# Performance work log

Hardware: AMD Instinct MI355X
Metric: run time of the kernel (lower is better)

The kernel has to match this reference:

```python
import jax, jax.numpy as jnp
import numpy as np

N = 50000
E = 800000
DF = 8        # dim_feat
DH = 32       # dim_hidden = out_channels per head
H = 4         # heads
HC = H * DH
DE = 4        # edge_dim
DD = 256      # dim_dense
DO = 4        # dim_out
NL = 3        # num GAT layers
SLOPE = 0.2   # GAT negative_slope
NL_SLOPE = 0.01  # nn.LeakyReLU default


def setup_inputs() -> dict:
    key = jax.random.key(0)
    ks = jax.random.split(key, 32)
    p = lambda k, shp: (jax.random.normal(k, shp, dtype=jnp.float32) * 0.1)
    inp = {
        "x": jax.random.normal(ks[0], (N, DF), dtype=jnp.float32),
        "edge_index": jax.random.randint(ks[1], (2, E), 0, N, dtype=jnp.int64),
        "edge_attr": jax.random.normal(ks[2], (E, DE), dtype=jnp.float32),
        # layer 0 (in = DF)
        "Wl0": p(ks[3], (DF, HC)), "bl0": jnp.zeros((HC,), jnp.float32),
        "Wr0": p(ks[4], (DF, HC)), "br0": jnp.zeros((HC,), jnp.float32),
        "We0": p(ks[5], (DE, HC)),
        "att0": p(ks[6], (H, DH)),
        "bo0": jnp.zeros((DH,), jnp.float32),
        # layers 1..NL-1 stacked (in = DH)
        "Wl": p(ks[7], (NL - 1, DH, HC)), "bl": jnp.zeros((NL - 1, HC), jnp.float32),
        "Wr": p(ks[8], (NL - 1, DH, HC)), "br": jnp.zeros((NL - 1, HC), jnp.float32),
        "We": p(ks[9], (NL - 1, DE, HC)),
        "att": p(ks[10], (NL - 1, H, DH)),
        "bo": jnp.zeros((NL - 1, DH), jnp.float32),
        # MLP head
        "Wd1": p(ks[11], (DH, DD)), "bd1": jnp.zeros((DD,), jnp.float32),
        "Wd2": p(ks[12], (DD, DO)), "bd2": jnp.zeros((DO,), jnp.float32),
    }
    return inp


def gat_layer(x, src, dst, ea, Wl, bl, Wr, br, We, att, bo):
    # GATv2ConvNorm, concat=False, no self loops, eval (dropout off)
    xl = (x @ Wl + bl).reshape(-1, H, DH)   # source transform  [N,H,C]
    xr = (x @ Wr + br).reshape(-1, H, DH)   # target transform  [N,H,C]
    x_j = xl[src]                            # [E,H,C]
    x_i = xr[dst]                            # [E,H,C]
    ef = (ea @ We).reshape(-1, H, DH)        # [E,H,C]
    m = jax.nn.leaky_relu(x_i + x_j + ef, negative_slope=SLOPE)
    e = jnp.einsum('ehc,hc->eh', m, att)     # logits [E,H]
    # Lipschitz norm on logits
    ni = jnp.linalg.norm(x_i, axis=-1)       # [E,H]
    nj = jnp.linalg.norm(x_j, axis=-1)       # [E,H]
    mx = jax.ops.segment_max(nj, dst, num_segments=N)
    mx = jnp.where(jnp.isfinite(mx), mx, 0.0)  # empty groups -> 0 (torch include_self=False init)
    e = e / (4.0 * (ni + mx[dst]) + 1e-12)
    # scatter softmax over destination groups
    emax = jax.ops.segment_max(e, dst, num_segments=N)
    z = jnp.exp(e - emax[dst])
    s = jax.ops.segment_sum(z, dst, num_segments=N)
    alpha = z / (s[dst] + 1e-16)             # [E,H]
    out = jax.ops.segment_sum(alpha[..., None] * x_j, dst, num_segments=N)  # [N,H,C]
    return out.mean(axis=1) + bo             # concat=False -> mean over heads


def reference(x, edge_index, edge_attr, Wl0, bl0, Wr0, br0, We0, att0, bo0,
              Wl, bl, Wr, br, We, att, bo, Wd1, bd1, Wd2, bd2):
    src, dst = edge_index[0], edge_index[1]
    act = lambda a: jax.nn.leaky_relu(a, negative_slope=NL_SLOPE)
    h = act(gat_layer(x, src, dst, edge_attr, Wl0, bl0, Wr0, br0, We0, att0, bo0))
    for i in range(NL - 1):
        h = act(gat_layer(h, src, dst, edge_attr, Wl[i], bl[i], Wr[i], br[i], We[i], att[i], bo[i]))
    h = act(h @ Wd1 + bd1)
    return h @ Wd2 + bd2
```

## Files before the change

### kernel.cpp

```cpp
#include <hip/hip_runtime.h>
#include <hip/hip_fp16.h>
#include <math.h>

#define NN 50000
#define EE 800000
#define DFi 8
#define DHc 32
#define Hh 4
#define HCc 128
#define DEe 4
#define DDd 256
#define DOo 4

__global__ void detect_kernel(const unsigned int* __restrict__ w, int nwords, int* __restrict__ flag) {
    unsigned int acc = 0;
    for (int i = 2 * threadIdx.x + 1; i < nwords; i += 512) acc |= w[i];
    if (acc) atomicOr(flag, 1);
}

__global__ void convert_count_kernel(const void* __restrict__ buf, const int* __restrict__ flag,
                                     int* __restrict__ EI, int* __restrict__ counts) {
    int i = blockIdx.x * 256 + threadIdx.x;
    if (i >= 2 * EE) return;
    int v = (*flag) ? ((const int*)buf)[i] : (int)(((const long long*)buf)[i]);
    EI[i] = v;
    if (i >= EE) atomicAdd(&counts[v], 1);
}

__global__ void scanA_kernel(const int* __restrict__ counts, int* __restrict__ roff,
                             int* __restrict__ bsum, int M) {
    __shared__ int sd[256];
    int t = threadIdx.x;
    int idx = blockIdx.x * 256 + t;
    int v = (idx < M) ? counts[idx] : 0;
    sd[t] = v;
    __syncthreads();
    for (int off = 1; off < 256; off <<= 1) {
        int x = (t >= off) ? sd[t - off] : 0;
        __syncthreads();
        sd[t] += x;
        __syncthreads();
    }
    if (idx < M) roff[idx] = sd[t] - v;
    if (t == 255) bsum[blockIdx.x] = sd[255];
}

__global__ void scanB_kernel(const int* __restrict__ bsum, int* __restrict__ boff, int nb) {
    __shared__ int sd[256];
    int t = threadIdx.x;
    int v = (t < nb) ? bsum[t] : 0;
    sd[t] = v;
    __syncthreads();
    for (int off = 1; off < 256; off <<= 1) {
        int x = (t >= off) ? sd[t - off] : 0;
        __syncthreads();
        sd[t] += x;
        __syncthreads();
    }
    boff[t] = sd[t] - v;
}

__global__ void scanC_kernel(int* __restrict__ roff, const int* __restrict__ boff, int M) {
    int idx = blockIdx.x * 256 + threadIdx.x;
    if (idx < M) roff[idx] += boff[idx >> 8];
}

__global__ void fill_kernel(const int* __restrict__ EI, const int* __restrict__ roff,
                            int* __restrict__ cursor, long long* __restrict__ ce) {
    int e = blockIdx.x * 256 + threadIdx.x;
    if (e >= EE) return;
    int d = EI[EE + e];
    int s = EI[e];
    int pos = atomicAdd(&cursor[d], 1);
    ce[roff[d] + pos] = ((long long)e << 32) | (unsigned int)s;
}

__global__ __launch_bounds__(256) void sortw_kernel(const int* __restrict__ roff,
                                                    long long* __restrict__ ce,
                                                    const float4* __restrict__ EA4,
                                                    int* __restrict__ col,
                                                    __half* __restrict__ EAc) {
    const int n = blockIdx.x * 4 + (threadIdx.x >> 6);
    if (n >= NN) return;
    const int lane = threadIdx.x & 63;
    const int a = roff[n];
    const int d = roff[n + 1] - a;
    if (d <= 0) return;
    if (d <= 64) {
        int srcv = 0;
        unsigned key = 0xFFFFFFFFu;
        if (lane < d) {
            long long v = ce[a + lane];
            srcv = (int)(v & 0xffffffffLL);
            unsigned eid = (unsigned)(v >> 32);
            key = (eid << 6) | (unsigned)lane;
        }
#pragma unroll
        for (int k = 2; k <= 64; k <<= 1) {
#pragma unroll
            for (int j = k >> 1; j > 0; j >>= 1) {
                unsigned o = (unsigned)__shfl_xor((int)key, j);
                bool up = ((lane & k) == 0);
                bool lower = ((lane & j) == 0);
                unsigned mn = o < key ? o : key;
                unsigned mx = o < key ? key : o;
                key = (lower == up) ? mn : mx;
            }
        }
        if (lane < d) {
            int ol = (int)(key & 63u);
            int src = __shfl(srcv, ol);
            unsigned eid = key >> 6;
            col[a + lane] = src;
            float4 at = EA4[eid];
            __half2 lo = __floats2half2_rn(at.x, at.y);
            __half2 hi = __floats2half2_rn(at.z, at.w);
            uint2 pk;
            pk.x = *reinterpret_cast<unsigned int*>(&lo);
            pk.y = *reinterpret_cast<unsigned int*>(&hi);
            reinterpret_cast<uint2*>(EAc)[a + lane] = pk;
        }
    } else if (lane == 0) {
        for (int i2 = a + 1; i2 < a + d; i2++) {
            long long kk = ce[i2];
            int j2 = i2 - 1;
            while (j2 >= a && ce[j2] > kk) { ce[j2 + 1] = ce[j2]; j2--; }
            ce[j2 + 1] = kk;
        }
        for (int k = 0; k < d; k++) {
            long long key = ce[a + k];
            int src = (int)(key & 0xffffffffLL);
            int eid = (int)(key >> 32);
            col[a + k] = src;
            float4 at = EA4[eid];
            __half2 lo = __floats2half2_rn(at.x, at.y);
            __half2 hi = __floats2half2_rn(at.z, at.w);
            uint2 pk;
            pk.x = *reinterpret_cast<unsigned int*>(&lo);
            pk.y = *reinterpret_cast<unsigned int*>(&hi);
            reinterpret_cast<uint2*>(EAc)[a + k] = pk;
        }
    }
}

template <int IN>
__global__ __launch_bounds__(128) void transform_kernel(
    const float* __restrict__ Xin, const float* __restrict__ Wl, const float* __restrict__ bl,
    const float* __restrict__ Wr, const float* __restrict__ br,
    __half* __restrict__ XLh, float* __restrict__ XR,
    float* __restrict__ NLn, float* __restrict__ NRn) {
    const int t = threadIdx.x;
    float wl[IN], wr[IN];
#pragma unroll
    for (int k = 0; k < IN; k++) { wl[k] = Wl[k * HCc + t]; wr[k] = Wr[k * HCc + t]; }
    const float blv = bl[t], brv = br[t];
    __shared__ float xst[16][IN];
    const int nbeg = blockIdx.x * 16;
    for (int idx = t; idx < 16 * IN; idx += 128) {
        int r = idx / IN, cc = idx % IN;
        int n = nbeg + r;
        xst[r][cc] = (n < NN) ? Xin[n * IN + cc] : 0.f;
    }
    __syncthreads();
#pragma unroll 4
    for (int r = 0; r < 16; ++r) {
        int n = nbeg + r;
        if (n >= NN) break;
        float al = blv, ar = brv;
#pragma unroll
        for (int k = 0; k < IN; k++) { float xv = xst[r][k]; al = fmaf(xv, wl[k], al); ar = fmaf(xv, wr[k], ar); }
        XLh[n * HCc + t] = __float2half(al);
        XR[n * HCc + t] = ar;
        float sl = al * al, sr = ar * ar;
#pragma unroll
        for (int msk = 1; msk < 32; msk <<= 1) { sl += __shfl_xor(sl, msk); sr += __shfl_xor(sr, msk); }
        if ((t & 31) == 0) { NLn[n * 4 + (t >> 5)] = sqrtf(sl); NRn[n * 4 + (t >> 5)] = sqrtf(sr); }
    }
}

__device__ inline float4 h8tof4(unsigned int a, unsigned int b) {
    __half2 p0 = *reinterpret_cast<const __half2*>(&a);
    __half2 p1 = *reinterpret_cast<const __half2*>(&b);
    float2 lo = __half22float2(p0), hi = __half22float2(p1);
    return make_float4(lo.x, lo.y, hi.x, hi.y);
}

__global__ __launch_bounds__(256) void gat_kernel(
    const __half* __restrict__ XLh, const float* __restrict__ XR,
    const float* __restrict__ NLn, const float* __restrict__ NRn,
    const int* __restrict__ roff, const int* __restrict__ col,
    const __half* __restrict__ EAc, const float* __restrict__ We,
    const float* __restrict__ att, const float* __restrict__ bo,
    float* __restrict__ Hout) {
    const int lane = threadIdx.x & 63;
    const int c = lane & 15;
    const int g = lane >> 4;
    const int h = c >> 2;
    const int wslot = blockIdx.x * 4 + (threadIdx.x >> 6);
    const int NWn = gridDim.x * 16;

    const uint4*  XLu4 = reinterpret_cast<const uint4*>(XLh);
    const uint2*  EAu2 = reinterpret_cast<const uint2*>(EAc);
    const float4* XR4 = reinterpret_cast<const float4*>(XR);
    const float4* NL4 = reinterpret_cast<const float4*>(NLn);
    const float4* We4 = reinterpret_cast<const float4*>(We);
    const float4* at4 = reinterpret_cast<const float4*>(att);
    const float4* bo4 = reinterpret_cast<const float4*>(bo);
    float4* Ho4 = reinterpret_cast<float4*>(Hout);

    const float4 w0l = We4[2 * c],      w0h = We4[2 * c + 1];
    const float4 w1l = We4[32 + 2 * c], w1h = We4[32 + 2 * c + 1];
    const float4 w2l = We4[64 + 2 * c], w2h = We4[64 + 2 * c + 1];
    const float4 w3l = We4[96 + 2 * c], w3h = We4[96 + 2 * c + 1];
    const float4 atl = at4[2 * c],      ath = at4[2 * c + 1];

    for (int i = wslot * 4 + g; i < NN; i += NWn) {
        const int base = roff[i];
        const int deg = roff[i + 1] - base;

        if (deg == 0) {
            if (c < 8) {
                float4 b = bo4[c];
                float4 r;
                r.x = b.x > 0.f ? b.x : 0.01f * b.x;
                r.y = b.y > 0.f ? b.y : 0.01f * b.y;
                r.z = b.z > 0.f ? b.z : 0.01f * b.z;
                r.w = b.w > 0.f ? b.w : 0.01f * b.w;
                Ho4[i * 8 + c] = r;
            }
            continue;
        }

        const float4 xil = XR4[i * 32 + 2 * c], xih = XR4[i * 32 + 2 * c + 1];
        float srun = 0.f;
        float4 accl = make_float4(0.f, 0.f, 0.f, 0.f);
        float4 acch = make_float4(0.f, 0.f, 0.f, 0.f);

#define ISSUE(X_, E_, K)                                                          \
        {                                                                         \
            int kc = ((K) < deg) ? (K) : 0;                                       \
            int jx = col[base + kc];                                              \
            X_ = XLu4[jx * 16 + c];                                               \
            E_ = EAu2[base + kc];                                                 \
        }
        uint4 xA, xB, xC, xD, xE, xF;
        uint2 eA, eB, eC, eD, eE, eF;
        ISSUE(xA, eA, 0); ISSUE(xB, eB, 1); ISSUE(xC, eC, 2);
        ISSUE(xD, eD, 3); ISSUE(xE, eE, 4); ISSUE(xF, eF, 5);

        float4 mx = make_float4(0.f, 0.f, 0.f, 0.f);
        for (int k = c; k < deg; k += 16) {
            int j = col[base + k];
            float4 nj = NL4[j];
            mx.x = fmaxf(mx.x, nj.x); mx.y = fmaxf(mx.y, nj.y);
            mx.z = fmaxf(mx.z, nj.z); mx.w = fmaxf(mx.w, nj.w);
        }
#pragma unroll
        for (int msk = 1; msk < 16; msk <<= 1) {
            mx.x = fmaxf(mx.x, __shfl_xor(mx.x, msk));
            mx.y = fmaxf(mx.y, __shfl_xor(mx.y, msk));
            mx.z = fmaxf(mx.z, __shfl_xor(mx.z, msk));
            mx.w = fmaxf(mx.w, __shfl_xor(mx.w, msk));
        }
        float mxh = (h == 0) ? mx.x : (h == 1) ? mx.y : (h == 2) ? mx.z : mx.w;
        const float invD = 1.0f / (4.0f * (NRn[i * 4 + h] + mxh) + 1e-12f);

#define BODY(X_, E_, K)                                                           \
        {                                                                         \
            float4 a4 = h8tof4((E_).x, (E_).y);                                   \
            float4 xjl = h8tof4((X_).x, (X_).y);                                  \
            float4 xjh = h8tof4((X_).z, (X_).w);                                  \
            float e0 = a4.x * w0l.x; e0 = fmaf(a4.y, w1l.x, e0);                  \
            e0 = fmaf(a4.z, w2l.x, e0); e0 = fmaf(a4.w, w3l.x, e0);               \
            float e1 = a4.x * w0l.y; e1 = fmaf(a4.y, w1l.y, e1);                  \
            e1 = fmaf(a4.z, w2l.y, e1); e1 = fmaf(a4.w, w3l.y, e1);               \
            float e2 = a4.x * w0l.z; e2 = fmaf(a4.y, w1l.z, e2);                  \
            e2 = fmaf(a4.z, w2l.z, e2); e2 = fmaf(a4.w, w3l.z, e2);               \
            float e3 = a4.x * w0l.w; e3 = fmaf(a4.y, w1l.w, e3);                  \
            e3 = fmaf(a4.z, w2l.w, e3); e3 = fmaf(a4.w, w3l.w, e3);               \
            float e4 = a4.x * w0h.x; e4 = fmaf(a4.y, w1h.x, e4);                  \
            e4 = fmaf(a4.z, w2h.x, e4); e4 = fmaf(a4.w, w3h.x, e4);               \
            float e5 = a4.x * w0h.y; e5 = fmaf(a4.y, w1h.y, e5);                  \
            e5 = fmaf(a4.z, w2h.y, e5); e5 = fmaf(a4.w, w3h.y, e5);               \
            float e6 = a4.x * w0h.z; e6 = fmaf(a4.y, w1h.z, e6);                  \
            e6 = fmaf(a4.z, w2h.z, e6); e6 = fmaf(a4.w, w3h.z, e6);               \
            float e7 = a4.x * w0h.w; e7 = fmaf(a4.y, w1h.w, e7);                  \
            e7 = fmaf(a4.z, w2h.w, e7); e7 = fmaf(a4.w, w3h.w, e7);               \
            float s0 = xil.x + xjl.x + e0; s0 = s0 > 0.f ? s0 : 0.2f * s0;        \
            float s1 = xil.y + xjl.y + e1; s1 = s1 > 0.f ? s1 : 0.2f * s1;        \
            float s2 = xil.z + xjl.z + e2; s2 = s2 > 0.f ? s2 : 0.2f * s2;        \
            float s3 = xil.w + xjl.w + e3; s3 = s3 > 0.f ? s3 : 0.2f * s3;        \
            float s4 = xih.x + xjh.x + e4; s4 = s4 > 0.f ? s4 : 0.2f * s4;        \
            float s5 = xih.y + xjh.y + e5; s5 = s5 > 0.f ? s5 : 0.2f * s5;        \
            float s6 = xih.z + xjh.z + e6; s6 = s6 > 0.f ? s6 : 0.2f * s6;        \
            float s7 = xih.w + xjh.w + e7; s7 = s7 > 0.f ? s7 : 0.2f * s7;        \
            float pp = s0 * atl.x; pp = fmaf(s1, atl.y, pp);                      \
            pp = fmaf(s2, atl.z, pp); pp = fmaf(s3, atl.w, pp);                   \
            pp = fmaf(s4, ath.x, pp); pp = fmaf(s5, ath.y, pp);                   \
            pp = fmaf(s6, ath.z, pp); pp = fmaf(s7, ath.w, pp);                   \
            pp += __shfl_xor(pp, 1); pp += __shfl_xor(pp, 2);                     \
            float z = __expf(fminf(pp * invD, 60.f));                             \
            z = ((K) < deg) ? z : 0.f;                                            \
            srun += z;                                                            \
            accl.x = fmaf(z, xjl.x, accl.x);                                      \
            accl.y = fmaf(z, xjl.y, accl.y);                                      \
            accl.z = fmaf(z, xjl.z, accl.z);                                      \
            accl.w = fmaf(z, xjl.w, accl.w);                                      \
            acch.x = fmaf(z, xjh.x, acch.x);                                      \
            acch.y = fmaf(z, xjh.y, acch.y);                                      \
            acch.z = fmaf(z, xjh.z, acch.z);                                      \
            acch.w = fmaf(z, xjh.w, acch.w);                                      \
        }

        for (int k = 0; k < deg; k += 3) {
            uint4 nxD, nxE, nxF;
            uint2 neD, neE, neF;
            ISSUE(nxD, neD, k + 6);
            ISSUE(nxE, neE, k + 7);
            ISSUE(nxF, neF, k + 8);
            BODY(xA, eA, k);
            if (k + 1 < deg) BODY(xB, eB, k + 1);
            if (k + 2 < deg) BODY(xC, eC, k + 2);
            xA = xD; eA = eD; xB = xE; eB = eE; xC = xF; eC = eF;
            xD = nxD; eD = neD; xE = nxE; eE = neE; xF = nxF; eF = neF;
        }
#undef BODY
#undef ISSUE

        float inv = 1.0f / (srun + 1e-16f);
        float a0 = accl.x * inv, a1 = accl.y * inv, a2 = accl.z * inv, a3 = accl.w * inv;
        float a4_ = acch.x * inv, a5 = acch.y * inv, a6 = acch.z * inv, a7 = acch.w * inv;
        a0 += __shfl_xor(a0, 4); a0 += __shfl_xor(a0, 8);
        a1 += __shfl_xor(a1, 4); a1 += __shfl_xor(a1, 8);
        a2 += __shfl_xor(a2, 4); a2 += __shfl_xor(a2, 8);
        a3 += __shfl_xor(a3, 4); a3 += __shfl_xor(a3, 8);
        a4_ += __shfl_xor(a4_, 4); a4_ += __shfl_xor(a4_, 8);
        a5 += __shfl_xor(a5, 4); a5 += __shfl_xor(a5, 8);
        a6 += __shfl_xor(a6, 4); a6 += __shfl_xor(a6, 8);
        a7 += __shfl_xor(a7, 4); a7 += __shfl_xor(a7, 8);

        if (c < 4) {
            float4 bl_ = bo4[2 * c], bh_ = bo4[2 * c + 1];
            float4 rl, rh;
            rl.x = fmaf(0.25f, a0, bl_.x); rl.x = rl.x > 0.f ? rl.x : 0.01f * rl.x;
            rl.y = fmaf(0.25f, a1, bl_.y); rl.y = rl.y > 0.f ? rl.y : 0.01f * rl.y;
            rl.z = fmaf(0.25f, a2, bl_.z); rl.z = rl.z > 0.f ? rl.z : 0.01f * rl.z;
            rl.w = fmaf(0.25f, a3, bl_.w); rl.w = rl.w > 0.f ? rl.w : 0.01f * rl.w;
            rh.x = fmaf(0.25f, a4_, bh_.x); rh.x = rh.x > 0.f ? rh.x : 0.01f * rh.x;
            rh.y = fmaf(0.25f, a5, bh_.y); rh.y = rh.y > 0.f ? rh.y : 0.01f * rh.y;
            rh.z = fmaf(0.25f, a6, bh_.z); rh.z = rh.z > 0.f ? rh.z : 0.01f * rh.z;
            rh.w = fmaf(0.25f, a7, bh_.w); rh.w = rh.w > 0.f ? rh.w : 0.01f * rh.w;
            Ho4[i * 8 + 2 * c] = rl;
            Ho4[i * 8 + 2 * c + 1] = rh;
        }
    }
}

__global__ __launch_bounds__(256) void mlp_kernel(
    const float* __restrict__ Hin, const float* __restrict__ Wd1, const float* __restrict__ bd1,
    const float* __restrict__ Wd2, const float* __restrict__ bd2, float* __restrict__ out) {
    const int lane = threadIdx.x & 63;
    const int chunk = __builtin_amdgcn_readfirstlane(threadIdx.x >> 6);
    const int nb = blockIdx.x * 64;
    int node = nb + lane;
    int nclamp = node < NN ? node : NN - 1;

    float h[32];
    const float4* H4 = reinterpret_cast<const float4*>(Hin);
#pragma unroll
    for (int r = 0; r < 8; ++r) {
        float4 t = H4[nclamp * 8 + r];
        h[4 * r] = t.x; h[4 * r + 1] = t.y; h[4 * r + 2] = t.z; h[4 * r + 3] = t.w;
    }

    float o0 = 0.f, o1 = 0.f, o2 = 0.f, o3 = 0.f;
    const int dbase = chunk * 64;
    for (int t = 0; t < 4; ++t) {
        float acc[16];
#pragma unroll
        for (int j = 0; j < 16; ++j) acc[j] = bd1[dbase + t * 16 + j];
#pragma unroll 8
        for (int k = 0; k < 32; ++k) {
            const float* wr = Wd1 + k * DDd + dbase + t * 16;
#pragma unroll
            for (int j = 0; j < 16; ++j) acc[j] = fmaf(h[k], wr[j], acc[j]);
        }
#pragma unroll
        for (int j = 0; j < 16; ++j) {
            float hd = acc[j];
            hd = hd > 0.f ? hd : 0.01f * hd;
            int d = dbase + t * 16 + j;
            o0 = fmaf(hd, Wd2[d * 4 + 0], o0);
            o1 = fmaf(hd, Wd2[d * 4 + 1], o1);
            o2 = fmaf(hd, Wd2[d * 4 + 2], o2);
            o3 = fmaf(hd, Wd2[d * 4 + 3], o3);
        }
    }

    __shared__ float4 red[4][64];
    red[chunk][lane] = make_float4(o0, o1, o2, o3);
    __syncthreads();
    if (threadIdx.x < 64 && nb + (int)threadIdx.x < NN) {
        float4 r0 = red[0][threadIdx.x], r1 = red[1][threadIdx.x];
        float4 r2 = red[2][threadIdx.x], r3 = red[3][threadIdx.x];
        float4 o;
        o.x = r0.x + r1.x + r2.x + r3.x + bd2[0];
        o.y = r0.y + r1.y + r2.y + r3.y + bd2[1];
        o.z = r0.z + r1.z + r2.z + r3.z + bd2[2];
        o.w = r0.w + r1.w + r2.w + r3.w + bd2[3];
        reinterpret_cast<float4*>(out)[nb + threadIdx.x] = o;
    }
}

extern "C" void kernel_launch(void* const* d_in, const int* in_sizes, int n_in,
                              void* d_out, int out_size, void* d_ws, size_t ws_size,
                              hipStream_t stream) {
    const float* x    = (const float*)d_in[0];
    const void*  eraw = d_in[1];
    const float* ea   = (const float*)d_in[2];
    const float* Wl0  = (const float*)d_in[3];
    const float* bl0  = (const float*)d_in[4];
    const float* Wr0  = (const float*)d_in[5];
    const float* br0  = (const float*)d_in[6];
    const float* We0  = (const float*)d_in[7];
    const float* att0 = (const float*)d_in[8];
    const float* bo0  = (const float*)d_in[9];
    const float* Wl   = (const float*)d_in[10];
    const float* bl   = (const float*)d_in[11];
    const float* Wr   = (const float*)d_in[12];
    const float* br   = (const float*)d_in[13];
    const float* We   = (const float*)d_in[14];
    const float* att  = (const float*)d_in[15];
    const float* bo   = (const float*)d_in[16];
    const float* Wd1  = (const float*)d_in[17];
    const float* bd1  = (const float*)d_in[18];
    const float* Wd2  = (const float*)d_in[19];
    const float* bd2  = (const float*)d_in[20];
    float* out = (float*)d_out;

    char* p = (char*)d_ws;
    auto alloc = [&](size_t bytes) { void* r = (void*)p; p += (bytes + 255) & ~(size_t)255; return r; };
    int*       EI     = (int*)alloc((size_t)2 * EE * 4);
    int*       counts = (int*)alloc((size_t)(NN + 1) * 4);
    int*       roff   = (int*)alloc((size_t)(NN + 1) * 4);
    int*       bsum   = (int*)alloc(256 * 4);
    int*       boff   = (int*)alloc(256 * 4);
    int*       cursor = (int*)alloc((size_t)NN * 4);
    long long* ce     = (long long*)alloc((size_t)EE * 8);
    int*       col    = (int*)alloc((size_t)EE * 4);
    int*       flag   = (int*)alloc(256);
    __half*    XLh    = (__half*)alloc((size_t)NN * HCc * 2);
    __half*    EAc    = (__half*)alloc((size_t)EE * 4 * 2);
    float*     XRb    = (float*)alloc((size_t)NN * HCc * 4);
    float*     NLn    = (float*)alloc((size_t)NN * 4 * 4);
    float*     NRn    = (float*)alloc((size_t)NN * 4 * 4);
    float*     HA     = (float*)alloc((size_t)NN * DHc * 4);
    float*     HB     = (float*)alloc((size_t)NN * DHc * 4);

    (void)hipMemsetAsync(counts, 0, (size_t)(NN + 1) * 4, stream);
    (void)hipMemsetAsync(cursor, 0, (size_t)NN * 4, stream);
    (void)hipMemsetAsync(flag, 0, 4, stream);

    detect_kernel<<<1, 256, 0, stream>>>((const unsigned int*)eraw, 8192, flag);
    convert_count_kernel<<<(2 * EE + 255) / 256, 256, 0, stream>>>(eraw, flag, EI, counts);
    const int M = NN + 1;
    const int NBLK = (M + 255) / 256;
    scanA_kernel<<<NBLK, 256, 0, stream>>>(counts, roff, bsum, M);
    scanB_kernel<<<1, 256, 0, stream>>>(bsum, boff, NBLK);
    scanC_kernel<<<NBLK, 256, 0, stream>>>(roff, boff, M);
    fill_kernel<<<(EE + 255) / 256, 256, 0, stream>>>(EI, roff, cursor, ce);
    sortw_kernel<<<(NN + 3) / 4, 256, 0, stream>>>(roff, ce, (const float4*)ea, col, EAc);

    const int gT = (NN + 15) / 16;
    const int gG = 1563;

    transform_kernel<DFi><<<gT, 128, 0, stream>>>(x, Wl0, bl0, Wr0, br0, XLh, XRb, NLn, NRn);
    gat_kernel<<<gG, 256, 0, stream>>>(XLh, XRb, NLn, NRn, roff, col, EAc, We0, att0, bo0, HA);
    transform_kernel<DHc><<<gT, 128, 0, stream>>>(HA, Wl, bl, Wr, br, XLh, XRb, NLn, NRn);
    gat_kernel<<<gG, 256, 0, stream>>>(XLh, XRb, NLn, NRn, roff, col, EAc, We, att, bo, HB);
    transform_kernel<DHc><<<gT, 128, 0, stream>>>(HB, Wl + DHc * HCc, bl + HCc, Wr + DHc * HCc, br + HCc,
                                                  XLh, XRb, NLn, NRn);
    gat_kernel<<<gG, 256, 0, stream>>>(XLh, XRb, NLn, NRn, roff, col, EAc, We + DEe * HCc,
                                       att + Hh * DHc, bo + DHc, HA);
    mlp_kernel<<<(NN + 63) / 64, 256, 0, stream>>>(HA, Wd1, bd1, Wd2, bd2, out);
}
```

Before: 455.2 us.

## Sort nodes by in-degree and map one node per 16-lane group

```diff
diff --git a/kernel.cpp b/kernel.cpp
--- a/kernel.cpp
+++ b/kernel.cpp
@@ -143,6 +143,37 @@
     }
 }
 
+__global__ void dhist_kernel(const int* __restrict__ roff, int* __restrict__ dhist) {
+    int n = blockIdx.x * 256 + threadIdx.x;
+    if (n >= NN) return;
+    int d = roff[n + 1] - roff[n];
+    atomicAdd(&dhist[d < 255 ? d : 255], 1);
+}
+
+__global__ void dscan_kernel(const int* __restrict__ dhist, int* __restrict__ dcur) {
+    __shared__ int sd[256];
+    int t = threadIdx.x;
+    int v = dhist[t];
+    sd[t] = v;
+    __syncthreads();
+    for (int off = 1; off < 256; off <<= 1) {
+        int x = (t >= off) ? sd[t - off] : 0;
+        __syncthreads();
+        sd[t] += x;
+        __syncthreads();
+    }
+    dcur[t] = sd[t] - v;
+}
+
+__global__ void dscatter_kernel(const int* __restrict__ roff, int* __restrict__ dcur,
+                                int* __restrict__ perm) {
+    int n = blockIdx.x * 256 + threadIdx.x;
+    if (n >= NN) return;
+    int d = roff[n + 1] - roff[n];
+    int pos = atomicAdd(&dcur[d < 255 ? d : 255], 1);
+    perm[pos] = n;
+}
+
 template <int IN>
 __global__ __launch_bounds__(128) void transform_kernel(
     const float* __restrict__ Xin, const float* __restrict__ Wl, const float* __restrict__ bl,
@@ -189,15 +220,17 @@
     const __half* __restrict__ XLh, const float* __restrict__ XR,
     const float* __restrict__ NLn, const float* __restrict__ NRn,
     const int* __restrict__ roff, const int* __restrict__ col,
-    const __half* __restrict__ EAc, const float* __restrict__ We,
+    const __half* __restrict__ EAc, const int* __restrict__ perm,
+    const float* __restrict__ We,
     const float* __restrict__ att, const float* __restrict__ bo,
     float* __restrict__ Hout) {
     const int lane = threadIdx.x & 63;
     const int c = lane & 15;
     const int g = lane >> 4;
     const int h = c >> 2;
-    const int wslot = blockIdx.x * 4 + (threadIdx.x >> 6);
-    const int NWn = gridDim.x * 16;
+    const int slot = blockIdx.x * 16 + (threadIdx.x >> 6) * 4 + g;
+    if (slot >= NN) return;
+    const int i = perm[slot];
 
     const uint4*  XLu4 = reinterpret_cast<const uint4*>(XLh);
     const uint2*  EAu2 = reinterpret_cast<const uint2*>(EAc);
@@ -208,151 +241,149 @@
     const float4* bo4 = reinterpret_cast<const float4*>(bo);
     float4* Ho4 = reinterpret_cast<float4*>(Hout);
 
+    const int base = roff[i];
+    const int deg = roff[i + 1] - base;
+
+    if (deg == 0) {
+        if (c < 8) {
+            float4 b = bo4[c];
+            float4 r;
+            r.x = b.x > 0.f ? b.x : 0.01f * b.x;
+            r.y = b.y > 0.f ? b.y : 0.01f * b.y;
+            r.z = b.z > 0.f ? b.z : 0.01f * b.z;
+            r.w = b.w > 0.f ? b.w : 0.01f * b.w;
+            Ho4[i * 8 + c] = r;
+        }
+        return;
+    }
+
     const float4 w0l = We4[2 * c],      w0h = We4[2 * c + 1];
     const float4 w1l = We4[32 + 2 * c], w1h = We4[32 + 2 * c + 1];
     const float4 w2l = We4[64 + 2 * c], w2h = We4[64 + 2 * c + 1];
     const float4 w3l = We4[96 + 2 * c], w3h = We4[96 + 2 * c + 1];
     const float4 atl = at4[2 * c],      ath = at4[2 * c + 1];
 
-    for (int i = wslot * 4 + g; i < NN; i += NWn) {
-        const int base = roff[i];
-        const int deg = roff[i + 1] - base;
-
-        if (deg == 0) {
-            if (c < 8) {
-                float4 b = bo4[c];
-                float4 r;
-                r.x = b.x > 0.f ? b.x : 0.01f * b.x;
-                r.y = b.y > 0.f ? b.y : 0.01f * b.y;
-                r.z = b.z > 0.f ? b.z : 0.01f * b.z;
-                r.w = b.w > 0.f ? b.w : 0.01f * b.w;
-                Ho4[i * 8 + c] = r;
-            }
-            continue;
-        }
-
-        const float4 xil = XR4[i * 32 + 2 * c], xih = XR4[i * 32 + 2 * c + 1];
-        float srun = 0.f;
-        float4 accl = make_float4(0.f, 0.f, 0.f, 0.f);
-        float4 acch = make_float4(0.f, 0.f, 0.f, 0.f);
+    const float4 xil = XR4[i * 32 + 2 * c], xih = XR4[i * 32 + 2 * c + 1];
+    float srun = 0.f;
+    float4 accl = make_float4(0.f, 0.f, 0.f, 0.f);
+    float4 acch = make_float4(0.f, 0.f, 0.f, 0.f);
 
 #define ISSUE(X_, E_, K)                                                          \
-        {                                                                         \
-            int kc = ((K) < deg) ? (K) : 0;                                       \
-            int jx = col[base + kc];                                              \
-            X_ = XLu4[jx * 16 + c];                                               \
-            E_ = EAu2[base + kc];                                                 \
-        }
-        uint4 xA, xB, xC, xD, xE, xF;
-        uint2 eA, eB, eC, eD, eE, eF;
-        ISSUE(xA, eA, 0); ISSUE(xB, eB, 1); ISSUE(xC, eC, 2);
-        ISSUE(xD, eD, 3); ISSUE(xE, eE, 4); ISSUE(xF, eF, 5);
-
-        float4 mx = make_float4(0.f, 0.f, 0.f, 0.f);
-        for (int k = c; k < deg; k += 16) {
-            int j = col[base + k];
-            float4 nj = NL4[j];
-            mx.x = fmaxf(mx.x, nj.x); mx.y = fmaxf(mx.y, nj.y);
-            mx.z = fmaxf(mx.z, nj.z); mx.w = fmaxf(mx.w, nj.w);
-        }
-#pragma unroll
-        for (int msk = 1; msk < 16; msk <<= 1) {
-            mx.x = fmaxf(mx.x, __shfl_xor(mx.x, msk));
-            mx.y = fmaxf(mx.y, __shfl_xor(mx.y, msk));
-            mx.z = fmaxf(mx.z, __shfl_xor(mx.z, msk));
-            mx.w = fmaxf(mx.w, __shfl_xor(mx.w, msk));
-        }
-        float mxh = (h == 0) ? mx.x : (h == 1) ? mx.y : (h == 2) ? mx.z : mx.w;
-        const float invD = 1.0f / (4.0f * (NRn[i * 4 + h] + mxh) + 1e-12f);
+    {                                                                             \
+        int kc = ((K) < deg) ? (K) : 0;                                           \
+        int jx = col[base + kc];                                                  \
+        X_ = XLu4[jx * 16 + c];                                                   \
+        E_ = EAu2[base + kc];                                                     \
+    }
+    uint4 xA, xB, xC, xD, xE, xF;
+    uint2 eA, eB, eC, eD, eE, eF;
+    ISSUE(xA, eA, 0); ISSUE(xB, eB, 1); ISSUE(xC, eC, 2);
+    ISSUE(xD, eD, 3); ISSUE(xE, eE, 4); ISSUE(xF, eF, 5);
+
+    float4 mx = make_float4(0.f, 0.f, 0.f, 0.f);
+    for (int k = c; k < deg; k += 16) {
+        int j = col[base + k];
+        float4 nj = NL4[j];
+        mx.x = fmaxf(mx.x, nj.x); mx.y = fmaxf(mx.y, nj.y);
+        mx.z = fmaxf(mx.z, nj.z); mx.w = fmaxf(mx.w, nj.w);
+    }
+#pragma unroll
+    for (int msk = 1; msk < 16; msk <<= 1) {
+        mx.x = fmaxf(mx.x, __shfl_xor(mx.x, msk));
+        mx.y = fmaxf(mx.y, __shfl_xor(mx.y, msk));
+        mx.z = fmaxf(mx.z, __shfl_xor(mx.z, msk));
+        mx.w = fmaxf(mx.w, __shfl_xor(mx.w, msk));
+    }
+    float mxh = (h == 0) ? mx.x : (h == 1) ? mx.y : (h == 2) ? mx.z : mx.w;
+    const float invD = 1.0f / (4.0f * (NRn[i * 4 + h] + mxh) + 1e-12f);
 
 #define BODY(X_, E_, K)                                                           \
-        {                                                                         \
-            float4 a4 = h8tof4((E_).x, (E_).y);                                   \
-            float4 xjl = h8tof4((X_).x, (X_).y);                                  \
-            float4 xjh = h8tof4((X_).z, (X_).w);                                  \
-            float e0 = a4.x * w0l.x; e0 = fmaf(a4.y, w1l.x, e0);                  \
-            e0 = fmaf(a4.z, w2l.x, e0); e0 = fmaf(a4.w, w3l.x, e0);               \
-            float e1 = a4.x * w0l.y; e1 = fmaf(a4.y, w1l.y, e1);                  \
-            e1 = fmaf(a4.z, w2l.y, e1); e1 = fmaf(a4.w, w3l.y, e1);               \
-            float e2 = a4.x * w0l.z; e2 = fmaf(a4.y, w1l.z, e2);                  \
-            e2 = fmaf(a4.z, w2l.z, e2); e2 = fmaf(a4.w, w3l.z, e2);               \
-            float e3 = a4.x * w0l.w; e3 = fmaf(a4.y, w1l.w, e3);                  \
-            e3 = fmaf(a4.z, w2l.w, e3); e3 = fmaf(a4.w, w3l.w, e3);               \
-            float e4 = a4.x * w0h.x; e4 = fmaf(a4.y, w1h.x, e4);                  \
-            e4 = fmaf(a4.z, w2h.x, e4); e4 = fmaf(a4.w, w3h.x, e4);               \
-            float e5 = a4.x * w0h.y; e5 = fmaf(a4.y, w1h.y, e5);                  \
-            e5 = fmaf(a4.z, w2h.y, e5); e5 = fmaf(a4.w, w3h.y, e5);               \
-            float e6 = a4.x * w0h.z; e6 = fmaf(a4.y, w1h.z, e6);                  \
-            e6 = fmaf(a4.z, w2h.z, e6); e6 = fmaf(a4.w, w3h.z, e6);               \
-            float e7 = a4.x * w0h.w; e7 = fmaf(a4.y, w1h.w, e7);                  \
-            e7 = fmaf(a4.z, w2h.w, e7); e7 = fmaf(a4.w, w3h.w, e7);               \
-            float s0 = xil.x + xjl.x + e0; s0 = s0 > 0.f ? s0 : 0.2f * s0;        \
-            float s1 = xil.y + xjl.y + e1; s1 = s1 > 0.f ? s1 : 0.2f * s1;        \
-            float s2 = xil.z + xjl.z + e2; s2 = s2 > 0.f ? s2 : 0.2f * s2;        \
-            float s3 = xil.w + xjl.w + e3; s3 = s3 > 0.f ? s3 : 0.2f * s3;        \
-            float s4 = xih.x + xjh.x + e4; s4 = s4 > 0.f ? s4 : 0.2f * s4;        \
-            float s5 = xih.y + xjh.y + e5; s5 = s5 > 0.f ? s5 : 0.2f * s5;        \
-            float s6 = xih.z + xjh.z + e6; s6 = s6 > 0.f ? s6 : 0.2f * s6;        \
-            float s7 = xih.w + xjh.w + e7; s7 = s7 > 0.f ? s7 : 0.2f * s7;        \
-            float pp = s0 * atl.x; pp = fmaf(s1, atl.y, pp);                      \
-            pp = fmaf(s2, atl.z, pp); pp = fmaf(s3, atl.w, pp);                   \
-            pp = fmaf(s4, ath.x, pp); pp = fmaf(s5, ath.y, pp);                   \
-            pp = fmaf(s6, ath.z, pp); pp = fmaf(s7, ath.w, pp);                   \
-            pp += __shfl_xor(pp, 1); pp += __shfl_xor(pp, 2);                     \
-            float z = __expf(fminf(pp * invD, 60.f));                             \
-            z = ((K) < deg) ? z : 0.f;                                            \
-            srun += z;                                                            \
-            accl.x = fmaf(z, xjl.x, accl.x);                                      \
-            accl.y = fmaf(z, xjl.y, accl.y);                                      \
-            accl.z = fmaf(z, xjl.z, accl.z);                                      \
-            accl.w = fmaf(z, xjl.w, accl.w);                                      \
-            acch.x = fmaf(z, xjh.x, acch.x);                                      \
-            acch.y = fmaf(z, xjh.y, acch.y);                                      \
-            acch.z = fmaf(z, xjh.z, acch.z);                                      \
-            acch.w = fmaf(z, xjh.w, acch.w);                                      \
-        }
-
-        for (int k = 0; k < deg; k += 3) {
-            uint4 nxD, nxE, nxF;
-            uint2 neD, neE, neF;
-            ISSUE(nxD, neD, k + 6);
-            ISSUE(nxE, neE, k + 7);
-            ISSUE(nxF, neF, k + 8);
-            BODY(xA, eA, k);
-            if (k + 1 < deg) BODY(xB, eB, k + 1);
-            if (k + 2 < deg) BODY(xC, eC, k + 2);
-            xA = xD; eA = eD; xB = xE; eB = eE; xC = xF; eC = eF;
-            xD = nxD; eD = neD; xE = nxE; eE = neE; xF = nxF; eF = neF;
-        }
+    {                                                                             \
+        float4 a4 = h8tof4((E_).x, (E_).y);                                       \
+        float4 xjl = h8tof4((X_).x, (X_).y);                                      \
+        float4 xjh = h8tof4((X_).z, (X_).w);                                      \
+        float e0 = a4.x * w0l.x; e0 = fmaf(a4.y, w1l.x, e0);                      \
+        e0 = fmaf(a4.z, w2l.x, e0); e0 = fmaf(a4.w, w3l.x, e0);                   \
+        float e1 = a4.x * w0l.y; e1 = fmaf(a4.y, w1l.y, e1);                      \
+        e1 = fmaf(a4.z, w2l.y, e1); e1 = fmaf(a4.w, w3l.y, e1);                   \
+        float e2 = a4.x * w0l.z; e2 = fmaf(a4.y, w1l.z, e2);                      \
+        e2 = fmaf(a4.z, w2l.z, e2); e2 = fmaf(a4.w, w3l.z, e2);                   \
+        float e3 = a4.x * w0l.w; e3 = fmaf(a4.y, w1l.w, e3);                      \
+        e3 = fmaf(a4.z, w2l.w, e3); e3 = fmaf(a4.w, w3l.w, e3);                   \
+        float e4 = a4.x * w0h.x; e4 = fmaf(a4.y, w1h.x, e4);                      \
+        e4 = fmaf(a4.z, w2h.x, e4); e4 = fmaf(a4.w, w3h.x, e4);                   \
+        float e5 = a4.x * w0h.y; e5 = fmaf(a4.y, w1h.y, e5);                      \
+        e5 = fmaf(a4.z, w2h.y, e5); e5 = fmaf(a4.w, w3h.y, e5);                   \
+        float e6 = a4.x * w0h.z; e6 = fmaf(a4.y, w1h.z, e6);                      \
+        e6 = fmaf(a4.z, w2h.z, e6); e6 = fmaf(a4.w, w3h.z, e6);                   \
+        float e7 = a4.x * w0h.w; e7 = fmaf(a4.y, w1h.w, e7);                      \
+        e7 = fmaf(a4.z, w2h.w, e7); e7 = fmaf(a4.w, w3h.w, e7);                   \
+        float s0 = xil.x + xjl.x + e0; s0 = s0 > 0.f ? s0 : 0.2f * s0;            \
+        float s1 = xil.y + xjl.y + e1; s1 = s1 > 0.f ? s1 : 0.2f * s1;            \
+        float s2 = xil.z + xjl.z + e2; s2 = s2 > 0.f ? s2 : 0.2f * s2;            \
+        float s3 = xil.w + xjl.w + e3; s3 = s3 > 0.f ? s3 : 0.2f * s3;            \
+        float s4 = xih.x + xjh.x + e4; s4 = s4 > 0.f ? s4 : 0.2f * s4;            \
+        float s5 = xih.y + xjh.y + e5; s5 = s5 > 0.f ? s5 : 0.2f * s5;            \
+        float s6 = xih.z + xjh.z + e6; s6 = s6 > 0.f ? s6 : 0.2f * s6;            \
+        float s7 = xih.w + xjh.w + e7; s7 = s7 > 0.f ? s7 : 0.2f * s7;            \
+        float pp = s0 * atl.x; pp = fmaf(s1, atl.y, pp);                          \
+        pp = fmaf(s2, atl.z, pp); pp = fmaf(s3, atl.w, pp);                       \
+        pp = fmaf(s4, ath.x, pp); pp = fmaf(s5, ath.y, pp);                       \
+        pp = fmaf(s6, ath.z, pp); pp = fmaf(s7, ath.w, pp);                       \
+        pp += __shfl_xor(pp, 1); pp += __shfl_xor(pp, 2);                         \
+        float z = __expf(fminf(pp * invD, 60.f));                                 \
+        z = ((K) < deg) ? z : 0.f;                                                \
+        srun += z;                                                                \
+        accl.x = fmaf(z, xjl.x, accl.x);                                          \
+        accl.y = fmaf(z, xjl.y, accl.y);                                          \
+        accl.z = fmaf(z, xjl.z, accl.z);                                          \
+        accl.w = fmaf(z, xjl.w, accl.w);                                          \
+        acch.x = fmaf(z, xjh.x, acch.x);                                          \
+        acch.y = fmaf(z, xjh.y, acch.y);                                          \
+        acch.z = fmaf(z, xjh.z, acch.z);                                          \
+        acch.w = fmaf(z, xjh.w, acch.w);                                          \
+    }
+
+    for (int k = 0; k < deg; k += 3) {
+        uint4 nxD, nxE, nxF;
+        uint2 neD, neE, neF;
+        ISSUE(nxD, neD, k + 6);
+        ISSUE(nxE, neE, k + 7);
+        ISSUE(nxF, neF, k + 8);
+        BODY(xA, eA, k);
+        if (k + 1 < deg) BODY(xB, eB, k + 1);
+        if (k + 2 < deg) BODY(xC, eC, k + 2);
+        xA = xD; eA = eD; xB = xE; eB = eE; xC = xF; eC = eF;
+        xD = nxD; eD = neD; xE = nxE; eE = neE; xF = nxF; eF = neF;
+    }
 #undef BODY
 #undef ISSUE
 
-        float inv = 1.0f / (srun + 1e-16f);
-        float a0 = accl.x * inv, a1 = accl.y * inv, a2 = accl.z * inv, a3 = accl.w * inv;
-        float a4_ = acch.x * inv, a5 = acch.y * inv, a6 = acch.z * inv, a7 = acch.w * inv;
-        a0 += __shfl_xor(a0, 4); a0 += __shfl_xor(a0, 8);
-        a1 += __shfl_xor(a1, 4); a1 += __shfl_xor(a1, 8);
-        a2 += __shfl_xor(a2, 4); a2 += __shfl_xor(a2, 8);
-        a3 += __shfl_xor(a3, 4); a3 += __shfl_xor(a3, 8);
-        a4_ += __shfl_xor(a4_, 4); a4_ += __shfl_xor(a4_, 8);
-        a5 += __shfl_xor(a5, 4); a5 += __shfl_xor(a5, 8);
-        a6 += __shfl_xor(a6, 4); a6 += __shfl_xor(a6, 8);
-        a7 += __shfl_xor(a7, 4); a7 += __shfl_xor(a7, 8);
-
-        if (c < 4) {
-            float4 bl_ = bo4[2 * c], bh_ = bo4[2 * c + 1];
-            float4 rl, rh;
-            rl.x = fmaf(0.25f, a0, bl_.x); rl.x = rl.x > 0.f ? rl.x : 0.01f * rl.x;
-            rl.y = fmaf(0.25f, a1, bl_.y); rl.y = rl.y > 0.f ? rl.y : 0.01f * rl.y;
-            rl.z = fmaf(0.25f, a2, bl_.z); rl.z = rl.z > 0.f ? rl.z : 0.01f * rl.z;
-            rl.w = fmaf(0.25f, a3, bl_.w); rl.w = rl.w > 0.f ? rl.w : 0.01f * rl.w;
-            rh.x = fmaf(0.25f, a4_, bh_.x); rh.x = rh.x > 0.f ? rh.x : 0.01f * rh.x;
-            rh.y = fmaf(0.25f, a5, bh_.y); rh.y = rh.y > 0.f ? rh.y : 0.01f * rh.y;
-            rh.z = fmaf(0.25f, a6, bh_.z); rh.z = rh.z > 0.f ? rh.z : 0.01f * rh.z;
-            rh.w = fmaf(0.25f, a7, bh_.w); rh.w = rh.w > 0.f ? rh.w : 0.01f * rh.w;
-            Ho4[i * 8 + 2 * c] = rl;
-            Ho4[i * 8 + 2 * c + 1] = rh;
-        }
+    float inv = 1.0f / (srun + 1e-16f);
+    float a0 = accl.x * inv, a1 = accl.y * inv, a2 = accl.z * inv, a3 = accl.w * inv;
+    float a4_ = acch.x * inv, a5 = acch.y * inv, a6 = acch.z * inv, a7 = acch.w * inv;
+    a0 += __shfl_xor(a0, 4); a0 += __shfl_xor(a0, 8);
+    a1 += __shfl_xor(a1, 4); a1 += __shfl_xor(a1, 8);
+    a2 += __shfl_xor(a2, 4); a2 += __shfl_xor(a2, 8);
+    a3 += __shfl_xor(a3, 4); a3 += __shfl_xor(a3, 8);
+    a4_ += __shfl_xor(a4_, 4); a4_ += __shfl_xor(a4_, 8);
+    a5 += __shfl_xor(a5, 4); a5 += __shfl_xor(a5, 8);
+    a6 += __shfl_xor(a6, 4); a6 += __shfl_xor(a6, 8);
+    a7 += __shfl_xor(a7, 4); a7 += __shfl_xor(a7, 8);
+
+    if (c < 4) {
+        float4 bl_ = bo4[2 * c], bh_ = bo4[2 * c + 1];
+        float4 rl, rh;
+        rl.x = fmaf(0.25f, a0, bl_.x); rl.x = rl.x > 0.f ? rl.x : 0.01f * rl.x;
+        rl.y = fmaf(0.25f, a1, bl_.y); rl.y = rl.y > 0.f ? rl.y : 0.01f * rl.y;
+        rl.z = fmaf(0.25f, a2, bl_.z); rl.z = rl.z > 0.f ? rl.z : 0.01f * rl.z;
+        rl.w = fmaf(0.25f, a3, bl_.w); rl.w = rl.w > 0.f ? rl.w : 0.01f * rl.w;
+        rh.x = fmaf(0.25f, a4_, bh_.x); rh.x = rh.x > 0.f ? rh.x : 0.01f * rh.x;
+        rh.y = fmaf(0.25f, a5, bh_.y); rh.y = rh.y > 0.f ? rh.y : 0.01f * rh.y;
+        rh.z = fmaf(0.25f, a6, bh_.z); rh.z = rh.z > 0.f ? rh.z : 0.01f * rh.z;
+        rh.w = fmaf(0.25f, a7, bh_.w); rh.w = rh.w > 0.f ? rh.w : 0.01f * rh.w;
+        Ho4[i * 8 + 2 * c] = rl;
+        Ho4[i * 8 + 2 * c + 1] = rh;
     }
 }
 
@@ -449,6 +480,9 @@
     long long* ce     = (long long*)alloc((size_t)EE * 8);
     int*       col    = (int*)alloc((size_t)EE * 4);
     int*       flag   = (int*)alloc(256);
+    int*       dhist  = (int*)alloc(256 * 4);
+    int*       dcur   = (int*)alloc(256 * 4);
+    int*       perm   = (int*)alloc((size_t)NN * 4);
     __half*    XLh    = (__half*)alloc((size_t)NN * HCc * 2);
     __half*    EAc    = (__half*)alloc((size_t)EE * 4 * 2);
     float*     XRb    = (float*)alloc((size_t)NN * HCc * 4);
@@ -460,6 +494,7 @@
     (void)hipMemsetAsync(counts, 0, (size_t)(NN + 1) * 4, stream);
     (void)hipMemsetAsync(cursor, 0, (size_t)NN * 4, stream);
     (void)hipMemsetAsync(flag, 0, 4, stream);
+    (void)hipMemsetAsync(dhist, 0, 256 * 4, stream);
 
     detect_kernel<<<1, 256, 0, stream>>>((const unsigned int*)eraw, 8192, flag);
     convert_count_kernel<<<(2 * EE + 255) / 256, 256, 0, stream>>>(eraw, flag, EI, counts);
@@ -470,17 +505,21 @@
     scanC_kernel<<<NBLK, 256, 0, stream>>>(roff, boff, M);
     fill_kernel<<<(EE + 255) / 256, 256, 0, stream>>>(EI, roff, cursor, ce);
     sortw_kernel<<<(NN + 3) / 4, 256, 0, stream>>>(roff, ce, (const float4*)ea, col, EAc);
+    const int gN = (NN + 255) / 256;
+    dhist_kernel<<<gN, 256, 0, stream>>>(roff, dhist);
+    dscan_kernel<<<1, 256, 0, stream>>>(dhist, dcur);
+    dscatter_kernel<<<gN, 256, 0, stream>>>(roff, dcur, perm);
 
     const int gT = (NN + 15) / 16;
-    const int gG = 1563;
+    const int gG = (NN + 15) / 16;
 
     transform_kernel<DFi><<<gT, 128, 0, stream>>>(x, Wl0, bl0, Wr0, br0, XLh, XRb, NLn, NRn);
-    gat_kernel<<<gG, 256, 0, stream>>>(XLh, XRb, NLn, NRn, roff, col, EAc, We0, att0, bo0, HA);
+    gat_kernel<<<gG, 256, 0, stream>>>(XLh, XRb, NLn, NRn, roff, col, EAc, perm, We0, att0, bo0, HA);
     transform_kernel<DHc><<<gT, 128, 0, stream>>>(HA, Wl, bl, Wr, br, XLh, XRb, NLn, NRn);
-    gat_kernel<<<gG, 256, 0, stream>>>(XLh, XRb, NLn, NRn, roff, col, EAc, We, att, bo, HB);
+    gat_kernel<<<gG, 256, 0, stream>>>(XLh, XRb, NLn, NRn, roff, col, EAc, perm, We, att, bo, HB);
     transform_kernel<DHc><<<gT, 128, 0, stream>>>(HB, Wl + DHc * HCc, bl + HCc, Wr + DHc * HCc, br + HCc,
                                                   XLh, XRb, NLn, NRn);
-    gat_kernel<<<gG, 256, 0, stream>>>(XLh, XRb, NLn, NRn, roff, col, EAc, We + DEe * HCc,
+    gat_kernel<<<gG, 256, 0, stream>>>(XLh, XRb, NLn, NRn, roff, col, EAc, perm, We + DEe * HCc,
                                        att + Hh * DHc, bo + DHc, HA);
     mlp_kernel<<<(NN + 63) / 64, 256, 0, stream>>>(HA, Wd1, bd1, Wd2, bd2, out);
 }
```

New measurement: 686.0 us. 1.51x slower.
